# Kernel tuning notes

Hardware: AMD Instinct MI355X
Metric: run time of the kernel (lower is better)

The kernel has to match this reference:

```python
import jax, jax.numpy as jnp
import numpy as np

N = 50000      # nodes
E = 800000     # edges (before self loops)
IN = 128       # in_channels
HID = 64       # hidden_channels
HEADS = 4
NCLS = 2
NEG_SLOPE = 0.2
BN_EPS = 1e-5

# per-layer config: (in_dim, heads, out_c, concat)
LAYERS = [(IN, HEADS, HID, True), (HID*HEADS, HEADS, HID, True), (HID*HEADS, HEADS, HID, True), (HID*HEADS, 1, HID, False)]

def setup_inputs():
    key = jax.random.key(0)
    ks = iter(jax.random.split(key, 64))
    d = {}
    d['x'] = jax.random.normal(next(ks), (N, IN), dtype=jnp.float32)
    d['edge_index'] = jax.random.randint(next(ks), (2, E), 0, N, dtype=jnp.int64)
    for i, (inc, h, oc, concat) in enumerate(LAYERS):
        d[f'W{i}'] = jax.random.normal(next(ks), (inc, h*oc), dtype=jnp.float32) * (1.0/np.sqrt(inc))
        d[f'as{i}'] = jax.random.normal(next(ks), (h, oc), dtype=jnp.float32) * 0.1
        d[f'ad{i}'] = jax.random.normal(next(ks), (h, oc), dtype=jnp.float32) * 0.1
        bn_dim = h*oc if concat else oc
        d[f'b{i}'] = jnp.zeros((bn_dim,), dtype=jnp.float32)
        d[f'g{i}'] = jnp.ones((bn_dim,), dtype=jnp.float32)
        d[f'be{i}'] = jnp.zeros((bn_dim,), dtype=jnp.float32)
    d['hw1'] = jax.random.normal(next(ks), (HID, HID//2), dtype=jnp.float32) * (1.0/np.sqrt(HID))
    d['hb1'] = jnp.zeros((HID//2,), dtype=jnp.float32)
    d['hw2'] = jax.random.normal(next(ks), (HID//2, NCLS), dtype=jnp.float32) * (1.0/np.sqrt(HID//2))
    d['hb2'] = jnp.zeros((NCLS,), dtype=jnp.float32)
    return d

def _gat_layer(x, src, dst, W, a_src, a_dst, bias, heads, out_c, concat):
    n = x.shape[0]
    h = (x @ W).reshape(n, heads, out_c)                 # [N,H,C]
    asrc = jnp.einsum('nhc,hc->nh', h, a_src)            # [N,H]
    adst = jnp.einsum('nhc,hc->nh', h, a_dst)            # [N,H]
    e = asrc[src] + adst[dst]                            # [Etot,H]
    e = jax.nn.leaky_relu(e, NEG_SLOPE)
    # segment softmax over incoming edges of each dst node
    m = jax.ops.segment_max(e, dst, num_segments=n)
    m = jnp.where(jnp.isfinite(m), m, 0.0)
    ex = jnp.exp(e - m[dst])
    s = jax.ops.segment_sum(ex, dst, num_segments=n)
    alpha = ex / (s[dst] + 1e-16)                        # [Etot,H]
    msg = h[src] * alpha[:, :, None]                     # [Etot,H,C]
    out = jax.ops.segment_sum(msg, dst, num_segments=n)  # [N,H,C]
    out = out.reshape(n, heads*out_c) if concat else out.mean(axis=1)
    return out + bias

def _bn(x, g, b):
    mu = x.mean(axis=0)
    var = x.var(axis=0)
    return g * (x - mu) * jax.lax.rsqrt(var + BN_EPS) + b

def reference(x, edge_index,
              W0, as0, ad0, b0, g0, be0,
              W1, as1, ad1, b1, g1, be1,
              W2, as2, ad2, b2, g2, be2,
              W3, as3, ad3, b3, g3, be3,
              hw1, hb1, hw2, hb2):
    loop = jnp.arange(N, dtype=edge_index.dtype)
    src = jnp.concatenate([edge_index[0], loop])
    dst = jnp.concatenate([edge_index[1], loop])
    params = [(W0, as0, ad0, b0, g0, be0), (W1, as1, ad1, b1, g1, be1),
              (W2, as2, ad2, b2, g2, be2), (W3, as3, ad3, b3, g3, be3)]
    h = x
    for (inc, heads, oc, concat), (W, a_s, a_d, b, g, be) in zip(LAYERS, params):
        h = _gat_layer(h, src, dst, W, a_s, a_d, b, heads, oc, concat)
        h = _bn(h, g, be)
        h = jax.nn.relu(h)
    h = jax.nn.relu(h @ hw1 + hb1)
    return h @ hw2 + hb2
```

## Files before the change

kernel.cpp:

```cpp
#include <hip/hip_runtime.h>

typedef __attribute__((ext_vector_type(8))) short bf16x8;
typedef __attribute__((ext_vector_type(4))) float f32x4;

__device__ __forceinline__ float bf2f(unsigned short u) {
    union { unsigned int i; float f; } x;
    x.i = ((unsigned int)u) << 16;
    return x.f;
}
__device__ __forceinline__ unsigned short f2bf(float f) {
    union { float f; unsigned int i; } x;
    x.f = f;
    unsigned int r = x.i + 0x7fffu + ((x.i >> 16) & 1u);
    return (unsigned short)(r >> 16);
}
__device__ __forceinline__ float ldf(const void* p, int i, int f32m) {
    if (f32m) return ((const float*)p)[i];
    return bf2f(((const unsigned short*)p)[i]);
}
__device__ __forceinline__ void unpack2(unsigned int u, float& lo, float& hi) {
    union { unsigned int i; float f; } a, b;
    a.i = u << 16;
    b.i = u & 0xffff0000u;
    lo = a.f;
    hi = b.f;
}

__global__ void zero_kernel(int* p, int n) {
    int i = blockIdx.x * 256 + threadIdx.x;
    if (i < n) p[i] = 0;
}

__global__ void probe_kernel(const int* ei, const unsigned int* xw, int* meta) {
    if (threadIdx.x == 0 && blockIdx.x == 0) {
        int orv = 0;
        for (int k = 0; k < 64; k++) orv |= ei[2 * k + 1];
        meta[0] = (orv == 0) ? 1 : 0;
        int cnt = 0;
        for (int k = 0; k < 64; k++) {
            unsigned int w = xw[k];
            int e = (int)((w >> 23) & 0xffu);
            if (e >= 107 && e <= 140) cnt++;
        }
        meta[1] = (cnt >= 48) ? 1 : 0;
    }
}

__global__ void hist_kernel(const int* ei, const int* meta, int* cnt, int E, int N) {
    int e = blockIdx.x * 256 + threadIdx.x;
    if (e >= E) return;
    int d = meta[0] ? ei[2 * (E + e)] : ei[E + e];
    if ((unsigned)d >= (unsigned)N) d = 0;
    atomicAdd(&cnt[d], 1);
}

__global__ void __launch_bounds__(256) chunkred_kernel(const int* cnt, int* csum, int N) {
    __shared__ int red[256];
    int t = threadIdx.x;
    int idx = blockIdx.x * 256 + t;
    red[t] = (idx < N) ? cnt[idx] : 0;
    __syncthreads();
    for (int off = 128; off > 0; off >>= 1) {
        if (t < off) red[t] += red[t + off];
        __syncthreads();
    }
    if (t == 0) csum[blockIdx.x] = red[0];
}

__global__ void __launch_bounds__(256) scanc_kernel(const int* csum, int* cbase, int* offs,
                                                    int nch, int N) {
    __shared__ int part[256];
    int t = threadIdx.x;
    int v = (t < nch) ? csum[t] : 0;
    part[t] = v;
    __syncthreads();
    for (int off = 1; off < 256; off <<= 1) {
        int tv = (t >= off) ? part[t - off] : 0;
        __syncthreads();
        part[t] += tv;
        __syncthreads();
    }
    if (t < nch) cbase[t] = part[t] - v;
    if (t == nch - 1) offs[N] = part[t];
}

__global__ void __launch_bounds__(256) offs_kernel(const int* cnt, const int* cbase,
                                                   int* offs, int N) {
    __shared__ int part[256];
    int t = threadIdx.x;
    int idx = blockIdx.x * 256 + t;
    int v = (idx < N) ? cnt[idx] : 0;
    part[t] = v;
    __syncthreads();
    for (int off = 1; off < 256; off <<= 1) {
        int tv = (t >= off) ? part[t - off] : 0;
        __syncthreads();
        part[t] += tv;
        __syncthreads();
    }
    if (idx < N) offs[idx] = cbase[blockIdx.x] + part[t] - v;
}

__global__ void scatter_kernel(const int* ei, const int* meta, const int* offs,
                               int* fill, int* csr, int E, int N) {
    int e = blockIdx.x * 256 + threadIdx.x;
    if (e >= E) return;
    int is64 = meta[0];
    int sv = is64 ? ei[2 * e] : ei[e];
    int d  = is64 ? ei[2 * (E + e)] : ei[E + e];
    if ((unsigned)sv >= (unsigned)N) sv = 0;
    if ((unsigned)d  >= (unsigned)N) d  = 0;
    int pos = offs[d] + atomicAdd(&fill[d], 1);
    csr[pos] = sv;
}

__global__ void __launch_bounds__(256) wsplit_all(const void* W0, const void* W1,
                                                  const void* W2, const void* W3,
                                                  const int* meta,
                                                  unsigned short* h0, unsigned short* l0,
                                                  unsigned short* h1, unsigned short* l1,
                                                  unsigned short* h2, unsigned short* l2,
                                                  unsigned short* h3, unsigned short* l3) {
    int e = blockIdx.x * 256 + threadIdx.x;
    const void* W;
    unsigned short *hi, *lo;
    int K, shift, idx;
    if (e < 32768)       { W = W0; hi = h0; lo = l0; K = 128; shift = 8; idx = e; }
    else if (e < 98304)  { W = W1; hi = h1; lo = l1; K = 256; shift = 8; idx = e - 32768; }
    else if (e < 163840) { W = W2; hi = h2; lo = l2; K = 256; shift = 8; idx = e - 98304; }
    else if (e < 180224) { W = W3; hi = h3; lo = l3; K = 256; shift = 6; idx = e - 163840; }
    else return;
    int k = idx >> shift;
    int n = idx & ((1 << shift) - 1);
    float x = ldf(W, idx, meta[1]);
    unsigned short h = f2bf(x);
    hi[n * K + k] = h;
    lo[n * K + k] = f2bf(x - bf2f(h));
}

__global__ void __launch_bounds__(256) gemm_mfma(const void* Aptr, int a_is_input,
                                                 const float* bnscale, const float* bnshift,
                                                 int apply_bn,
                                                 const unsigned short* Bhi,
                                                 const unsigned short* Blo,
                                                 void* Cout, int out_bf16,
                                                 const void* aw_s, const void* aw_d,
                                                 float* asrc, float* adst,
                                                 int M, int K, int NC, const int* meta) {
    __shared__ unsigned short sAhi[64 * 40];
    __shared__ unsigned short sAlo[64 * 40];
    __shared__ unsigned short sBhi[64 * 40];
    __shared__ unsigned short sBlo[64 * 40];
    __shared__ float sScale[256];
    __shared__ float sShift[256];
    int wmode = meta[1];
    int amode = a_is_input ? wmode : 1;
    int t = threadIdx.x;
    int wid = t >> 6;
    int lane = t & 63;
    int row0 = blockIdx.x * 64;
    int col0 = blockIdx.y * 64;
    int H = NC >> 6;

    if (apply_bn && t < K) {
        sScale[t] = bnscale[t];
        sShift[t] = bnshift[t];
    }
    __syncthreads();

    int ar = t >> 2;
    int ak = (t & 3) * 8;

    f32x4 acc[4];
    #pragma unroll
    for (int i = 0; i < 4; i++) acc[i] = (f32x4){0.0f, 0.0f, 0.0f, 0.0f};

    int m = lane & 15;
    int q = lane >> 4;

    for (int kt = 0; kt < K; kt += 32) {
        {
            int gr = row0 + ar;
            float v[8];
            if (gr < M) {
                if (amode) {
                    const float* ap = (const float*)Aptr + (size_t)gr * K + kt + ak;
                    float4 f0 = *(const float4*)ap;
                    float4 f1 = *(const float4*)(ap + 4);
                    v[0] = f0.x; v[1] = f0.y; v[2] = f0.z; v[3] = f0.w;
                    v[4] = f1.x; v[5] = f1.y; v[6] = f1.z; v[7] = f1.w;
                } else {
                    const unsigned short* ap =
                        (const unsigned short*)Aptr + (size_t)gr * K + kt + ak;
                    uint4 u = *(const uint4*)ap;
                    unpack2(u.x, v[0], v[1]);
                    unpack2(u.y, v[2], v[3]);
                    unpack2(u.z, v[4], v[5]);
                    unpack2(u.w, v[6], v[7]);
                }
                if (apply_bn) {
                    #pragma unroll
                    for (int j = 0; j < 8; j++)
                        v[j] = fmaxf(fmaf(v[j], sScale[kt + ak + j], sShift[kt + ak + j]), 0.0f);
                }
            } else {
                #pragma unroll
                for (int j = 0; j < 8; j++) v[j] = 0.0f;
            }
            unsigned short h[8], l[8];
            #pragma unroll
            for (int j = 0; j < 8; j++) {
                h[j] = f2bf(v[j]);
                l[j] = f2bf(v[j] - bf2f(h[j]));
            }
            uint4 ho, lu;
            ho.x = (unsigned int)h[0] | ((unsigned int)h[1] << 16);
            ho.y = (unsigned int)h[2] | ((unsigned int)h[3] << 16);
            ho.z = (unsigned int)h[4] | ((unsigned int)h[5] << 16);
            ho.w = (unsigned int)h[6] | ((unsigned int)h[7] << 16);
            lu.x = (unsigned int)l[0] | ((unsigned int)l[1] << 16);
            lu.y = (unsigned int)l[2] | ((unsigned int)l[3] << 16);
            lu.z = (unsigned int)l[4] | ((unsigned int)l[5] << 16);
            lu.w = (unsigned int)l[6] | ((unsigned int)l[7] << 16);
            *(uint4*)(sAhi + ar * 40 + ak) = ho;
            *(uint4*)(sAlo + ar * 40 + ak) = lu;
            uint4 bh4 = *(const uint4*)(Bhi + (size_t)(col0 + ar) * K + kt + ak);
            uint4 bl4 = *(const uint4*)(Blo + (size_t)(col0 + ar) * K + kt + ak);
            *(uint4*)(sBhi + ar * 40 + ak) = bh4;
            *(uint4*)(sBlo + ar * 40 + ak) = bl4;
        }
        __syncthreads();

        bf16x8 ahi = *(const bf16x8*)(sAhi + (wid * 16 + m) * 40 + q * 8);
        bf16x8 alo = *(const bf16x8*)(sAlo + (wid * 16 + m) * 40 + q * 8);
        #pragma unroll
        for (int tn = 0; tn < 4; tn++) {
            bf16x8 bhi = *(const bf16x8*)(sBhi + (tn * 16 + m) * 40 + q * 8);
            bf16x8 blo = *(const bf16x8*)(sBlo + (tn * 16 + m) * 40 + q * 8);
            acc[tn] = __builtin_amdgcn_mfma_f32_16x16x32_bf16(ahi, bhi, acc[tn], 0, 0, 0);
            acc[tn] = __builtin_amdgcn_mfma_f32_16x16x32_bf16(alo, bhi, acc[tn], 0, 0, 0);
            acc[tn] = __builtin_amdgcn_mfma_f32_16x16x32_bf16(ahi, blo, acc[tn], 0, 0, 0);
        }
        __syncthreads();
    }

    #pragma unroll
    for (int tn = 0; tn < 4; tn++) {
        int gcol = col0 + tn * 16 + m;
        #pragma unroll
        for (int reg = 0; reg < 4; reg++) {
            int grow = row0 + wid * 16 + q * 4 + reg;
            if (grow < M) {
                if (out_bf16)
                    ((unsigned short*)Cout)[(size_t)grow * NC + gcol] = f2bf(acc[tn][reg]);
                else
                    ((float*)Cout)[(size_t)grow * NC + gcol] = acc[tn][reg];
            }
        }
    }

    float ps[4] = {0.f, 0.f, 0.f, 0.f};
    float pd[4] = {0.f, 0.f, 0.f, 0.f};
    #pragma unroll
    for (int tn = 0; tn < 4; tn++) {
        float asv = ldf(aw_s, blockIdx.y * 64 + tn * 16 + m, wmode);
        float adv = ldf(aw_d, blockIdx.y * 64 + tn * 16 + m, wmode);
        #pragma unroll
        for (int reg = 0; reg < 4; reg++) {
            ps[reg] = fmaf(acc[tn][reg], asv, ps[reg]);
            pd[reg] = fmaf(acc[tn][reg], adv, pd[reg]);
        }
    }
    #pragma unroll
    for (int reg = 0; reg < 4; reg++) {
        #pragma unroll
        for (int off = 1; off < 16; off <<= 1) {
            ps[reg] += __shfl_xor(ps[reg], off);
            pd[reg] += __shfl_xor(pd[reg], off);
        }
    }
    if (m == 0) {
        #pragma unroll
        for (int reg = 0; reg < 4; reg++) {
            int grow = row0 + wid * 16 + q * 4 + reg;
            if (grow < M) {
                asrc[grow * H + blockIdx.y] = ps[reg];
                adst[grow * H + blockIdx.y] = pd[reg];
            }
        }
    }
}

__global__ void __launch_bounds__(256) aggb4(const unsigned short* hfb, const float* asrc,
                                             const float* adst, const int* offs,
                                             const int* csr, float* out, int N) {
    int wid = threadIdx.x >> 6;
    int l = threadIdx.x & 63;
    int node = blockIdx.x * 4 + wid;
    if (node >= N) return;
    int h = l >> 4;
    int beg = offs[node], end = offs[node + 1];
    float ad = adst[node * 4 + h];
    float e0 = asrc[node * 4 + h] + ad;
    e0 = (e0 < 0.0f) ? 0.2f * e0 : e0;
    float w0 = __expf(e0);
    uint2 u0 = ((const uint2*)(hfb + (size_t)node * 256))[l];
    float g0a, g0b, g0c, g0d;
    unpack2(u0.x, g0a, g0b);
    unpack2(u0.y, g0c, g0d);
    float s = w0;
    float a0 = w0 * g0a, a1 = w0 * g0b, a2 = w0 * g0c, a3 = w0 * g0d;
    int i = beg;
    for (; i + 4 <= end; i += 4) {
        int s0 = csr[i], s1 = csr[i + 1], s2 = csr[i + 2], s3 = csr[i + 3];
        float e_0 = asrc[s0 * 4 + h] + ad;
        float e_1 = asrc[s1 * 4 + h] + ad;
        float e_2 = asrc[s2 * 4 + h] + ad;
        float e_3 = asrc[s3 * 4 + h] + ad;
        uint2 u_0 = ((const uint2*)(hfb + (size_t)s0 * 256))[l];
        uint2 u_1 = ((const uint2*)(hfb + (size_t)s1 * 256))[l];
        uint2 u_2 = ((const uint2*)(hfb + (size_t)s2 * 256))[l];
        uint2 u_3 = ((const uint2*)(hfb + (size_t)s3 * 256))[l];
        e_0 = (e_0 < 0.0f) ? 0.2f * e_0 : e_0;
        e_1 = (e_1 < 0.0f) ? 0.2f * e_1 : e_1;
        e_2 = (e_2 < 0.0f) ? 0.2f * e_2 : e_2;
        e_3 = (e_3 < 0.0f) ? 0.2f * e_3 : e_3;
        float wv0 = __expf(e_0), wv1 = __expf(e_1), wv2 = __expf(e_2), wv3 = __expf(e_3);
        s += (wv0 + wv1) + (wv2 + wv3);
        float x0, x1, x2, x3;
        unpack2(u_0.x, x0, x1); unpack2(u_0.y, x2, x3);
        a0 = fmaf(wv0, x0, a0); a1 = fmaf(wv0, x1, a1);
        a2 = fmaf(wv0, x2, a2); a3 = fmaf(wv0, x3, a3);
        unpack2(u_1.x, x0, x1); unpack2(u_1.y, x2, x3);
        a0 = fmaf(wv1, x0, a0); a1 = fmaf(wv1, x1, a1);
        a2 = fmaf(wv1, x2, a2); a3 = fmaf(wv1, x3, a3);
        unpack2(u_2.x, x0, x1); unpack2(u_2.y, x2, x3);
        a0 = fmaf(wv2, x0, a0); a1 = fmaf(wv2, x1, a1);
        a2 = fmaf(wv2, x2, a2); a3 = fmaf(wv2, x3, a3);
        unpack2(u_3.x, x0, x1); unpack2(u_3.y, x2, x3);
        a0 = fmaf(wv3, x0, a0); a1 = fmaf(wv3, x1, a1);
        a2 = fmaf(wv3, x2, a2); a3 = fmaf(wv3, x3, a3);
    }
    for (; i < end; i++) {
        int sn = csr[i];
        float es = asrc[sn * 4 + h] + ad;
        es = (es < 0.0f) ? 0.2f * es : es;
        float wv = __expf(es);
        uint2 u = ((const uint2*)(hfb + (size_t)sn * 256))[l];
        float x0, x1, x2, x3;
        unpack2(u.x, x0, x1); unpack2(u.y, x2, x3);
        s += wv;
        a0 = fmaf(wv, x0, a0); a1 = fmaf(wv, x1, a1);
        a2 = fmaf(wv, x2, a2); a3 = fmaf(wv, x3, a3);
    }
    float rs = 1.0f / (s + 1e-16f);
    float4 o;
    o.x = a0 * rs; o.y = a1 * rs; o.z = a2 * rs; o.w = a3 * rs;
    *(float4*)&out[(size_t)node * 256 + l * 4] = o;
}

__global__ void __launch_bounds__(256) aggf1(const float* hf, const float* asrc,
                                             const float* adst, const int* offs,
                                             const int* csr, float* out, int N) {
    int wid = threadIdx.x >> 6;
    int c = threadIdx.x & 63;
    int node = blockIdx.x * 4 + wid;
    if (node >= N) return;
    int beg = offs[node], end = offs[node + 1];
    float ad = adst[node];
    float e0 = asrc[node] + ad;
    e0 = (e0 < 0.0f) ? 0.2f * e0 : e0;
    float w0 = __expf(e0);
    float s = w0;
    float acc0 = w0 * hf[(size_t)node * 64 + c];
    float acc1 = 0.0f, acc2 = 0.0f, acc3 = 0.0f;
    int i = beg;
    for (; i + 4 <= end; i += 4) {
        int s0 = csr[i], s1 = csr[i + 1], s2 = csr[i + 2], s3 = csr[i + 3];
        float e_0 = asrc[s0] + ad;
        float e_1 = asrc[s1] + ad;
        float e_2 = asrc[s2] + ad;
        float e_3 = asrc[s3] + ad;
        float g0 = hf[(size_t)s0 * 64 + c];
        float g1 = hf[(size_t)s1 * 64 + c];
        float g2 = hf[(size_t)s2 * 64 + c];
        float g3 = hf[(size_t)s3 * 64 + c];
        e_0 = (e_0 < 0.0f) ? 0.2f * e_0 : e_0;
        e_1 = (e_1 < 0.0f) ? 0.2f * e_1 : e_1;
        e_2 = (e_2 < 0.0f) ? 0.2f * e_2 : e_2;
        e_3 = (e_3 < 0.0f) ? 0.2f * e_3 : e_3;
        float w0_ = __expf(e_0), w1_ = __expf(e_1), w2_ = __expf(e_2), w3_ = __expf(e_3);
        s += (w0_ + w1_) + (w2_ + w3_);
        acc0 = fmaf(w0_, g0, acc0);
        acc1 = fmaf(w1_, g1, acc1);
        acc2 = fmaf(w2_, g2, acc2);
        acc3 = fmaf(w3_, g3, acc3);
    }
    for (; i < end; i++) {
        int sn = csr[i];
        float es = asrc[sn] + ad;
        es = (es < 0.0f) ? 0.2f * es : es;
        float wv = __expf(es);
        s += wv;
        acc0 = fmaf(wv, hf[(size_t)sn * 64 + c], acc0);
    }
    float acc = (acc0 + acc1) + (acc2 + acc3);
    out[(size_t)node * 64 + c] = acc / (s + 1e-16f);
}

__global__ void __launch_bounds__(256) bnstats_kernel(const float* x, float* partial,
                                                      int N, int NC, int c4shift) {
    __shared__ float4 ls[256];
    __shared__ float4 lq[256];
    int t = threadIdx.x;
    int c4 = t & ((1 << c4shift) - 1);
    int rsub = t >> c4shift;
    int rstep = 256 >> c4shift;
    int r0 = blockIdx.x * 32 + rsub;
    int r1 = blockIdx.x * 32 + 32;
    if (r1 > N) r1 = N;
    float4 s = {0.f, 0.f, 0.f, 0.f}, q = {0.f, 0.f, 0.f, 0.f};
    for (int r = r0; r < r1; r += rstep) {
        float4 v = *(const float4*)(x + (size_t)r * NC + c4 * 4);
        s.x += v.x; s.y += v.y; s.z += v.z; s.w += v.w;
        q.x = fmaf(v.x, v.x, q.x);
        q.y = fmaf(v.y, v.y, q.y);
        q.z = fmaf(v.z, v.z, q.z);
        q.w = fmaf(v.w, v.w, q.w);
    }
    ls[t] = s;
    lq[t] = q;
    __syncthreads();
    for (int step = 128; step >= (1 << c4shift); step >>= 1) {
        if (t < step) {
            float4 a = ls[t + step], b = lq[t + step];
            ls[t].x += a.x; ls[t].y += a.y; ls[t].z += a.z; ls[t].w += a.w;
            lq[t].x += b.x; lq[t].y += b.y; lq[t].z += b.z; lq[t].w += b.w;
        }
        __syncthreads();
    }
    if (t < (1 << c4shift)) {
        *(float4*)(partial + (size_t)blockIdx.x * 2 * NC + t * 4) = ls[t];
        *(float4*)(partial + (size_t)blockIdx.x * 2 * NC + NC + t * 4) = lq[t];
    }
}

__global__ void __launch_bounds__(256) bnfinal(const float* partial, int nblk, const void* g,
                                               const void* be, float* scale, float* shift,
                                               int NC, float invN, const int* meta) {
    __shared__ float rs_[256];
    __shared__ float rq_[256];
    int t = threadIdx.x;
    int fl = t & 31;
    int rg = t >> 5;
    int f = blockIdx.x * 32 + fl;
    float s = 0.0f, q = 0.0f;
    for (int b = rg; b < nblk; b += 8) {
        s += partial[(size_t)b * 2 * NC + f];
        q += partial[(size_t)b * 2 * NC + NC + f];
    }
    rs_[t] = s;
    rq_[t] = q;
    __syncthreads();
    for (int step = 128; step >= 32; step >>= 1) {
        if (t < step) {
            rs_[t] += rs_[t + step];
            rq_[t] += rq_[t + step];
        }
        __syncthreads();
    }
    if (t < 32) {
        int wmode = meta[1];
        float mu = rs_[t] * invN;
        float var = rq_[t] * invN - mu * mu;
        if (var < 0.0f) var = 0.0f;
        float rsq = rsqrtf(var + 1e-5f);
        float sc = ldf(g, f, wmode) * rsq;
        scale[f] = sc;
        shift[f] = ldf(be, f, wmode) - mu * sc;
    }
}

__global__ void __launch_bounds__(256) head_kernel(const float* xin, const float* bnscale,
                                                   const float* bnshift, const void* hw1,
                                                   const void* hb1, const void* hw2,
                                                   const void* hb2, void* out, int N,
                                                   const int* meta) {
    __shared__ float w1[64 * 32];
    __shared__ float w2[64];
    __shared__ float b1[32];
    __shared__ float b2[2];
    __shared__ float sc[64];
    __shared__ float sh[64];
    int wmode = meta[1];
    for (int i = threadIdx.x; i < 2048; i += 256) w1[i] = ldf(hw1, i, wmode);
    if (threadIdx.x < 64) {
        w2[threadIdx.x] = ldf(hw2, threadIdx.x, wmode);
        sc[threadIdx.x] = bnscale[threadIdx.x];
        sh[threadIdx.x] = bnshift[threadIdx.x];
    }
    if (threadIdx.x < 32) b1[threadIdx.x] = ldf(hb1, threadIdx.x, wmode);
    if (threadIdx.x < 2) b2[threadIdx.x] = ldf(hb2, threadIdx.x, wmode);
    __syncthreads();
    int n = blockIdx.x * 256 + threadIdx.x;
    if (n >= N) return;
    float x[64];
    for (int i = 0; i < 64; i++)
        x[i] = fmaxf(fmaf(xin[(size_t)n * 64 + i], sc[i], sh[i]), 0.0f);
    float o0 = b2[0], o1 = b2[1];
    for (int j = 0; j < 32; j++) {
        float a = b1[j];
        #pragma unroll
        for (int k = 0; k < 64; k++) a = fmaf(x[k], w1[k * 32 + j], a);
        a = fmaxf(a, 0.0f);
        o0 = fmaf(a, w2[j * 2], o0);
        o1 = fmaf(a, w2[j * 2 + 1], o1);
    }
    if (wmode) {
        ((float*)out)[n * 2] = o0;
        ((float*)out)[n * 2 + 1] = o1;
    } else {
        ((unsigned short*)out)[n * 2] = f2bf(o0);
        ((unsigned short*)out)[n * 2 + 1] = f2bf(o1);
    }
}

extern "C" void kernel_launch(void* const* d_in, const int* in_sizes, int n_in,
                              void* d_out, int out_size, void* d_ws, size_t ws_size,
                              hipStream_t stream) {
    size_t out_bytes2 = (size_t)out_size * 2;

    if (n_in != 30 || in_sizes[0] != 50000 * 128 || in_sizes[1] != 2 * 800000 ||
        in_sizes[2] != 128 * 256 || in_sizes[26] != 64 * 32) {
        hipMemsetAsync(d_out, 0x4E, out_bytes2, stream);
        return;
    }

    const int N = 50000;
    const int E = 800000;

    const void* x_in = d_in[0];
    const int* ei = (const int*)d_in[1];
    const void* W0  = d_in[2];
    const void* As0 = d_in[3];
    const void* Ad0 = d_in[4];
    const void* G0  = d_in[6];
    const void* Be0 = d_in[7];
    const void* W1  = d_in[8];
    const void* As1 = d_in[9];
    const void* Ad1 = d_in[10];
    const void* G1  = d_in[12];
    const void* Be1 = d_in[13];
    const void* W2  = d_in[14];
    const void* As2 = d_in[15];
    const void* Ad2 = d_in[16];
    const void* G2  = d_in[18];
    const void* Be2 = d_in[19];
    const void* W3  = d_in[20];
    const void* As3 = d_in[21];
    const void* Ad3 = d_in[22];
    const void* G3  = d_in[24];
    const void* Be3 = d_in[25];
    const void* hw1 = d_in[26];
    const void* hb1 = d_in[27];
    const void* hw2 = d_in[28];
    const void* hb2 = d_in[29];

    char* base = (char*)d_ws;
    size_t off = 0;
    auto alloc = [&](size_t bytes) {
        void* r = (void*)(base + off);
        off += (bytes + 255) & ~(size_t)255;
        return r;
    };
    int nch = (N + 255) / 256;
    int nblkBN = (N + 31) / 32;
    int* meta    = (int*)alloc(256);
    int* cnt     = (int*)alloc((size_t)N * 4);
    int* fill    = (int*)alloc((size_t)N * 4);
    size_t zero_end = off;
    float* partial = (float*)alloc((size_t)nblkBN * 512 * 4);
    int* csum    = (int*)alloc(256 * 4);
    int* cbase   = (int*)alloc(256 * 4);
    int* offs    = (int*)alloc((size_t)(N + 1) * 4);
    int* csr     = (int*)alloc((size_t)E * 4);
    float* asrc  = (float*)alloc((size_t)N * 4 * 4);
    float* adst  = (float*)alloc((size_t)N * 4 * 4);
    float* scaleb = (float*)alloc(256 * 4);
    float* shiftb = (float*)alloc(256 * 4);
    unsigned short* hfb = (unsigned short*)alloc((size_t)N * 256 * 2);
    float* hff   = (float*)alloc((size_t)N * 64 * 4);
    float* xbuf  = (float*)alloc((size_t)N * 256 * 4);
    unsigned short* w0hi = (unsigned short*)alloc(128 * 256 * 2);
    unsigned short* w0lo = (unsigned short*)alloc(128 * 256 * 2);
    unsigned short* w1hi = (unsigned short*)alloc(256 * 256 * 2);
    unsigned short* w1lo = (unsigned short*)alloc(256 * 256 * 2);
    unsigned short* w2hi = (unsigned short*)alloc(256 * 256 * 2);
    unsigned short* w2lo = (unsigned short*)alloc(256 * 256 * 2);
    unsigned short* w3hi = (unsigned short*)alloc(256 * 64 * 2);
    unsigned short* w3lo = (unsigned short*)alloc(256 * 64 * 2);

    if (ws_size < off) {
        hipMemsetAsync(d_out, 0x4D, out_bytes2, stream);
        return;
    }

    int zn = (int)((zero_end - 256) / 4);
    zero_kernel<<<(zn + 255) / 256, 256, 0, stream>>>(cnt, zn);
    probe_kernel<<<1, 64, 0, stream>>>(ei, (const unsigned int*)x_in, meta);

    int gE = (E + 255) / 256;
    hist_kernel<<<gE, 256, 0, stream>>>(ei, meta, cnt, E, N);
    chunkred_kernel<<<nch, 256, 0, stream>>>(cnt, csum, N);
    scanc_kernel<<<1, 256, 0, stream>>>(csum, cbase, offs, nch, N);
    offs_kernel<<<nch, 256, 0, stream>>>(cnt, cbase, offs, N);
    scatter_kernel<<<gE, 256, 0, stream>>>(ei, meta, offs, fill, csr, E, N);

    wsplit_all<<<(180224 + 255) / 256, 256, 0, stream>>>(
        W0, W1, W2, W3, meta, w0hi, w0lo, w1hi, w1lo, w2hi, w2lo, w3hi, w3lo);

    int gM64 = (N + 63) / 64;
    int gND = (N + 3) / 4;
    float invN = 1.0f / (float)N;

    const unsigned short* whi[4] = {w0hi, w1hi, w2hi, w3hi};
    const unsigned short* wlo[4] = {w0lo, w1lo, w2lo, w3lo};
    const void* Asl[4] = {As0, As1, As2, As3};
    const void* Adl[4] = {Ad0, Ad1, Ad2, Ad3};
    const void* Gl[4]  = {G0, G1, G2, G3};
    const void* Bel[4] = {Be0, Be1, Be2, Be3};

    for (int L = 0; L < 3; L++) {
        if (L == 0)
            gemm_mfma<<<dim3(gM64, 4), 256, 0, stream>>>(
                x_in, 1, scaleb, shiftb, 0, whi[L], wlo[L], hfb, 1,
                Asl[L], Adl[L], asrc, adst, N, 128, 256, meta);
        else
            gemm_mfma<<<dim3(gM64, 4), 256, 0, stream>>>(
                xbuf, 0, scaleb, shiftb, 1, whi[L], wlo[L], hfb, 1,
                Asl[L], Adl[L], asrc, adst, N, 256, 256, meta);
        aggb4<<<gND, 256, 0, stream>>>(hfb, asrc, adst, offs, csr, xbuf, N);
        bnstats_kernel<<<nblkBN, 256, 0, stream>>>(xbuf, partial, N, 256, 6);
        bnfinal<<<8, 256, 0, stream>>>(partial, nblkBN, Gl[L], Bel[L],
                                       scaleb, shiftb, 256, invN, meta);
    }

    gemm_mfma<<<dim3(gM64, 1), 256, 0, stream>>>(
        xbuf, 0, scaleb, shiftb, 1, w3hi, w3lo, hff, 0,
        As3, Ad3, asrc, adst, N, 256, 64, meta);
    aggf1<<<gND, 256, 0, stream>>>(hff, asrc, adst, offs, csr, xbuf, N);
    bnstats_kernel<<<nblkBN, 256, 0, stream>>>(xbuf, partial, N, 64, 4);
    bnfinal<<<2, 256, 0, stream>>>(partial, nblkBN, G3, Be3, scaleb, shiftb, 64, invN, meta);

    head_kernel<<<(N + 255) / 256, 256, 0, stream>>>(xbuf, scaleb, shiftb, hw1, hb1, hw2, hb2,
                                                     d_out, N, meta);
}
```

Measured before the change: 904.4 us.

## Compute full 256-column output per block in GAT layer GEMM

```diff
diff --git a/kernel.cpp b/kernel.cpp
--- a/kernel.cpp
+++ b/kernel.cpp
@@ -136,6 +136,161 @@
     unsigned short h = f2bf(x);
     hi[n * K + k] = h;
     lo[n * K + k] = f2bf(x - bf2f(h));
+}
+
+__global__ void __launch_bounds__(256) gemm_mfma256(const void* Aptr, int a_is_input,
+                                                    const float* bnscale, const float* bnshift,
+                                                    int apply_bn,
+                                                    const unsigned short* Bhi,
+                                                    const unsigned short* Blo,
+                                                    unsigned short* Cout,
+                                                    const void* aw_s, const void* aw_d,
+                                                    float* asrc, float* adst,
+                                                    int M, int K, const int* meta) {
+    __shared__ unsigned short sAhi[64 * 40];
+    __shared__ unsigned short sAlo[64 * 40];
+    __shared__ unsigned short sBhi[256 * 40];
+    __shared__ unsigned short sBlo[256 * 40];
+    __shared__ float sScale[256];
+    __shared__ float sShift[256];
+    int wmode = meta[1];
+    int amode = a_is_input ? wmode : 1;
+    int t = threadIdx.x;
+    int wid = t >> 6;
+    int lane = t & 63;
+    int row0 = blockIdx.x * 64;
+
+    if (apply_bn && t < K) {
+        sScale[t] = bnscale[t];
+        sShift[t] = bnshift[t];
+    }
+    __syncthreads();
+
+    int ar = t >> 2;
+    int ak = (t & 3) * 8;
+
+    f32x4 acc[16];
+    #pragma unroll
+    for (int i = 0; i < 16; i++) acc[i] = (f32x4){0.0f, 0.0f, 0.0f, 0.0f};
+
+    int m = lane & 15;
+    int q = lane >> 4;
+
+    for (int kt = 0; kt < K; kt += 32) {
+        {
+            int gr = row0 + ar;
+            float v[8];
+            if (gr < M) {
+                if (amode) {
+                    const float* ap = (const float*)Aptr + (size_t)gr * K + kt + ak;
+                    float4 f0 = *(const float4*)ap;
+                    float4 f1 = *(const float4*)(ap + 4);
+                    v[0] = f0.x; v[1] = f0.y; v[2] = f0.z; v[3] = f0.w;
+                    v[4] = f1.x; v[5] = f1.y; v[6] = f1.z; v[7] = f1.w;
+                } else {
+                    const unsigned short* ap =
+                        (const unsigned short*)Aptr + (size_t)gr * K + kt + ak;
+                    uint4 u = *(const uint4*)ap;
+                    unpack2(u.x, v[0], v[1]);
+                    unpack2(u.y, v[2], v[3]);
+                    unpack2(u.z, v[4], v[5]);
+                    unpack2(u.w, v[6], v[7]);
+                }
+                if (apply_bn) {
+                    #pragma unroll
+                    for (int j = 0; j < 8; j++)
+                        v[j] = fmaxf(fmaf(v[j], sScale[kt + ak + j], sShift[kt + ak + j]), 0.0f);
+                }
+            } else {
+                #pragma unroll
+                for (int j = 0; j < 8; j++) v[j] = 0.0f;
+            }
+            unsigned short h[8], l[8];
+            #pragma unroll
+            for (int j = 0; j < 8; j++) {
+                h[j] = f2bf(v[j]);
+                l[j] = f2bf(v[j] - bf2f(h[j]));
+            }
+            uint4 ho, lu;
+            ho.x = (unsigned int)h[0] | ((unsigned int)h[1] << 16);
+            ho.y = (unsigned int)h[2] | ((unsigned int)h[3] << 16);
+            ho.z = (unsigned int)h[4] | ((unsigned int)h[5] << 16);
+            ho.w = (unsigned int)h[6] | ((unsigned int)h[7] << 16);
+            lu.x = (unsigned int)l[0] | ((unsigned int)l[1] << 16);
+            lu.y = (unsigned int)l[2] | ((unsigned int)l[3] << 16);
+            lu.z = (unsigned int)l[4] | ((unsigned int)l[5] << 16);
+            lu.w = (unsigned int)l[6] | ((unsigned int)l[7] << 16);
+            *(uint4*)(sAhi + ar * 40 + ak) = ho;
+            *(uint4*)(sAlo + ar * 40 + ak) = lu;
+        }
+        {
+            const unsigned short* bh = Bhi + (size_t)t * K + kt;
+            const unsigned short* bl = Blo + (size_t)t * K + kt;
+            #pragma unroll
+            for (int j = 0; j < 4; j++) {
+                *(uint4*)(sBhi + t * 40 + j * 8) = *(const uint4*)(bh + j * 8);
+                *(uint4*)(sBlo + t * 40 + j * 8) = *(const uint4*)(bl + j * 8);
+            }
+        }
+        __syncthreads();
+
+        bf16x8 ahi = *(const bf16x8*)(sAhi + (wid * 16 + m) * 40 + q * 8);
+        bf16x8 alo = *(const bf16x8*)(sAlo + (wid * 16 + m) * 40 + q * 8);
+        #pragma unroll
+        for (int tn = 0; tn < 16; tn++) {
+            bf16x8 bhi = *(const bf16x8*)(sBhi + (tn * 16 + m) * 40 + q * 8);
+            bf16x8 blo = *(const bf16x8*)(sBlo + (tn * 16 + m) * 40 + q * 8);
+            acc[tn] = __builtin_amdgcn_mfma_f32_16x16x32_bf16(ahi, bhi, acc[tn], 0, 0, 0);
+            acc[tn] = __builtin_amdgcn_mfma_f32_16x16x32_bf16(alo, bhi, acc[tn], 0, 0, 0);
+            acc[tn] = __builtin_amdgcn_mfma_f32_16x16x32_bf16(ahi, blo, acc[tn], 0, 0, 0);
+        }
+        __syncthreads();
+    }
+
+    #pragma unroll
+    for (int tn = 0; tn < 16; tn++) {
+        int gcol = tn * 16 + m;
+        #pragma unroll
+        for (int reg = 0; reg < 4; reg++) {
+            int grow = row0 + wid * 16 + q * 4 + reg;
+            if (grow < M)
+                Cout[(size_t)grow * 256 + gcol] = f2bf(acc[tn][reg]);
+        }
+    }
+
+    for (int hh = 0; hh < 4; hh++) {
+        float ps[4] = {0.f, 0.f, 0.f, 0.f};
+        float pd[4] = {0.f, 0.f, 0.f, 0.f};
+        #pragma unroll
+        for (int tq = 0; tq < 4; tq++) {
+            int tn = hh * 4 + tq;
+            float asv = ldf(aw_s, tn * 16 + m, wmode);
+            float adv = ldf(aw_d, tn * 16 + m, wmode);
+            #pragma unroll
+            for (int reg = 0; reg < 4; reg++) {
+                ps[reg] = fmaf(acc[tn][reg], asv, ps[reg]);
+                pd[reg] = fmaf(acc[tn][reg], adv, pd[reg]);
+            }
+        }
+        #pragma unroll
+        for (int reg = 0; reg < 4; reg++) {
+            #pragma unroll
+            for (int off = 1; off < 16; off <<= 1) {
+                ps[reg] += __shfl_xor(ps[reg], off);
+                pd[reg] += __shfl_xor(pd[reg], off);
+            }
+        }
+        if (m == 0) {
+            #pragma unroll
+            for (int reg = 0; reg < 4; reg++) {
+                int grow = row0 + wid * 16 + q * 4 + reg;
+                if (grow < M) {
+                    asrc[grow * 4 + hh] = ps[reg];
+                    adst[grow * 4 + hh] = pd[reg];
+                }
+            }
+        }
+    }
 }
 
 __global__ void __launch_bounds__(256) gemm_mfma(const void* Aptr, int a_is_input,
@@ -632,13 +787,13 @@
 
     for (int L = 0; L < 3; L++) {
         if (L == 0)
-            gemm_mfma<<<dim3(gM64, 4), 256, 0, stream>>>(
-                x_in, 1, scaleb, shiftb, 0, whi[L], wlo[L], hfb, 1,
-                Asl[L], Adl[L], asrc, adst, N, 128, 256, meta);
+            gemm_mfma256<<<gM64, 256, 0, stream>>>(
+                x_in, 1, scaleb, shiftb, 0, whi[L], wlo[L], hfb,
+                Asl[L], Adl[L], asrc, adst, N, 128, meta);
         else
-            gemm_mfma<<<dim3(gM64, 4), 256, 0, stream>>>(
-                xbuf, 0, scaleb, shiftb, 1, whi[L], wlo[L], hfb, 1,
-                Asl[L], Adl[L], asrc, adst, N, 256, 256, meta);
+            gemm_mfma256<<<gM64, 256, 0, stream>>>(
+                xbuf, 0, scaleb, shiftb, 1, whi[L], wlo[L], hfb,
+                Asl[L], Adl[L], asrc, adst, N, 256, meta);
         aggb4<<<gND, 256, 0, stream>>>(hfb, asrc, adst, offs, csr, xbuf, N);
         bnstats_kernel<<<nblkBN, 256, 0, stream>>>(xbuf, partial, N, 256, 6);
         bnfinal<<<8, 256, 0, stream>>>(partial, nblkBN, Gl[L], Bel[L],
```

Result: slower. 936.0 us (+3.5%).
